# Optimization experiments

Measured on AMD Instinct MI355X. Metric: run time of the kernel, lower is better.

Reference implementation:

```python
import jax, jax.numpy as jnp
import numpy as np

N_HEADS = 16

def setup_inputs() -> dict:
    key = jax.random.key(0)
    k1, k2 = jax.random.split(key)
    qkv = jax.random.normal(k1, (4, 3072, 2048), dtype=jnp.float32)
    encoder_kv = jax.random.normal(k2, (4, 2048, 256), dtype=jnp.float32)
    return {"qkv": qkv, "encoder_kv": encoder_kv}

def reference(qkv, encoder_kv):
    bs, width, length = qkv.shape
    ch = width // (3 * N_HEADS)  # 64
    # [bs*H, 3*ch, T] -> q, k, v each [bs*H, ch, T]
    q, k, v = jnp.split(qkv.reshape(bs * N_HEADS, 3 * ch, length), 3, axis=1)
    # encoder kv: [bs, H*2*ch, S] -> ek, ev each [bs*H, ch, S]
    ek, ev = jnp.split(encoder_kv.reshape(bs * N_HEADS, 2 * ch, -1), 2, axis=1)
    k = jnp.concatenate([ek, k], axis=-1)  # [bs*H, ch, S+T]
    v = jnp.concatenate([ev, v], axis=-1)
    scale = ch ** -0.25  # 1/sqrt(sqrt(ch)), applied to both q and k
    weight = jnp.einsum('bct,bcs->bts', q * scale, k * scale)  # [bs*H, T, S+T]
    weight = jax.nn.softmax(weight.astype(jnp.float32), axis=-1).astype(qkv.dtype)
    a = jnp.einsum('bts,bcs->bct', weight, v)  # [bs*H, ch, T]
    return a.reshape(bs, -1, length)
```

## Files before the change

### kernel.cpp

```cpp
#include <hip/hip_runtime.h>
#include <hip/hip_bf16.h>

typedef __attribute__((ext_vector_type(8))) short bf16x8;
typedef __attribute__((ext_vector_type(4))) float f32x4;
typedef __attribute__((ext_vector_type(4))) unsigned u32x4;
typedef __attribute__((ext_vector_type(2))) unsigned u32x2;

#define T_LEN 2048
#define S_ENC 256
#define QSCALE 0.18033688011112042f

#define BARRIER()                                         \
  do {                                                    \
    asm volatile("s_waitcnt lgkmcnt(0)" ::: "memory");    \
    __builtin_amdgcn_s_barrier();                         \
  } while (0)

__device__ __forceinline__ float exp2_hw(float x) {
#if __has_builtin(__builtin_amdgcn_exp2f)
  return __builtin_amdgcn_exp2f(x);
#else
  float r;
  asm("v_exp_f32 %0, %1" : "=v"(r) : "v"(x));
  return r;
#endif
}

__device__ __forceinline__ unsigned cvt_pk_bf16(float lo, float hi) {
  unsigned r;
  asm("v_cvt_pk_bf16_f32 %0, %1, %2" : "=v"(r) : "v"(lo), "v"(hi));
  return r;
}

__device__ __forceinline__ short f2bf(float x) {
  union { __hip_bfloat16 b; short s; } u;
  u.b = __float2bfloat16(x);
  return u.s;
}

__device__ __forceinline__ int swz(int row, int col) {
  return row * 64 + (col ^ ((row & 7) << 3));
}

union PU { u32x4 u; bf16x8 b; };

template<int STRIDE>
__device__ __forceinline__ void tile_body(
    const float* __restrict__ kb, const float* __restrict__ vb, int s0,
    short* __restrict__ Kt, short* __restrict__ Vt,
    const bf16x8 (&qf)[2][2], f32x4 (&o)[2][4], float (&lp)[2], int tid) {

  const int lane = tid & 63;
  const int ln = lane & 15;
  const int lg = lane >> 4;

  const int ks = tid & 63;
  const int kc = (tid >> 6) * 8;
  float kr[8];
  const float* kp = kb + (size_t)kc * STRIDE + (s0 + ks);
#pragma unroll
  for (int r = 0; r < 8; ++r) kr[r] = kp[(size_t)r * STRIDE];

  const int vg = tid & 15;
  const int vc = tid >> 4;
  const float* vp0 = vb + (size_t)vc * STRIDE + (s0 + 4 * vg);
  f32x4 vr0 = *(const f32x4*)(vp0);
  f32x4 vr1 = *(const f32x4*)(vp0 + (size_t)32 * STRIDE);

  BARRIER();

  u32x4 kw;
#pragma unroll
  for (int r = 0; r < 4; ++r) kw[r] = cvt_pk_bf16(kr[2 * r], kr[2 * r + 1]);
  *(u32x4*)(Kt + swz(ks, kc)) = kw;

  const int vcol = 32 * (vg >> 3) + 8 * (vg & 3) + 4 * ((vg >> 2) & 1);
  u32x2 vw0, vw1;
  vw0[0] = cvt_pk_bf16(vr0[0], vr0[1]);
  vw0[1] = cvt_pk_bf16(vr0[2], vr0[3]);
  *(u32x2*)(Vt + swz(vc, vcol)) = vw0;
  vw1[0] = cvt_pk_bf16(vr1[0], vr1[1]);
  vw1[1] = cvt_pk_bf16(vr1[2], vr1[3]);
  *(u32x2*)(Vt + swz(vc + 32, vcol)) = vw1;

  BARRIER();

  f32x4 sacc[2][4];
#pragma unroll
  for (int qt = 0; qt < 2; ++qt)
#pragma unroll
    for (int mt = 0; mt < 4; ++mt) sacc[qt][mt] = (f32x4){0.f, 0.f, 0.f, 0.f};

#pragma unroll
  for (int mt = 0; mt < 4; ++mt) {
    const int row = 16 * mt + ln;
    const bf16x8 kf0 = *(const bf16x8*)(Kt + swz(row, 8 * lg));
    const bf16x8 kf1 = *(const bf16x8*)(Kt + swz(row, 32 + 8 * lg));
#pragma unroll
    for (int qt = 0; qt < 2; ++qt) {
      sacc[qt][mt] = __builtin_amdgcn_mfma_f32_16x16x32_bf16(kf0, qf[qt][0], sacc[qt][mt], 0, 0, 0);
      sacc[qt][mt] = __builtin_amdgcn_mfma_f32_16x16x32_bf16(kf1, qf[qt][1], sacc[qt][mt], 0, 0, 0);
    }
  }

  PU pfrag[2][2];
#pragma unroll
  for (int qt = 0; qt < 2; ++qt) {
    float pmt[4];
#pragma unroll
    for (int mt = 0; mt < 4; ++mt) {
      float p0 = exp2_hw(sacc[qt][mt][0]);
      float p1 = exp2_hw(sacc[qt][mt][1]);
      float p2 = exp2_hw(sacc[qt][mt][2]);
      float p3 = exp2_hw(sacc[qt][mt][3]);
      pfrag[qt][mt >> 1].u[2 * (mt & 1) + 0] = cvt_pk_bf16(p0, p1);
      pfrag[qt][mt >> 1].u[2 * (mt & 1) + 1] = cvt_pk_bf16(p2, p3);
      pmt[mt] = (p0 + p1) + (p2 + p3);
    }
    lp[qt] += (pmt[0] + pmt[1]) + (pmt[2] + pmt[3]);
  }

#pragma unroll
  for (int sub = 0; sub < 2; ++sub)
#pragma unroll
    for (int ct = 0; ct < 4; ++ct) {
      const bf16x8 vf = *(const bf16x8*)(Vt + swz(16 * ct + ln, 32 * sub + 8 * lg));
#pragma unroll
      for (int qt = 0; qt < 2; ++qt)
        o[qt][ct] = __builtin_amdgcn_mfma_f32_16x16x32_bf16(vf, pfrag[qt][sub].b, o[qt][ct], 0, 0, 0);
    }
}

__global__ __launch_bounds__(512, 4) void attn_kernel(
    const float* __restrict__ qkv, const float* __restrict__ ekv,
    float* __restrict__ out) {
  const int tid = threadIdx.x;
  const int lane = tid & 63;
  const int wave = tid >> 6;
  const int ln = lane & 15;
  const int lg = lane >> 4;

  const int bh = blockIdx.x & 63;
  const int qb = blockIdx.x >> 6;
  const int t0 = qb * 256 + wave * 32;

  const float* qp  = qkv + (size_t)bh * 192 * T_LEN;
  const float* kp  = qp + (size_t)64 * T_LEN;
  const float* vp  = qp + (size_t)128 * T_LEN;
  const float* ekp = ekv + (size_t)bh * 128 * S_ENC;
  const float* evp = ekp + (size_t)64 * S_ENC;

  __shared__ __attribute__((aligned(16))) short Kt[64 * 64];
  __shared__ __attribute__((aligned(16))) short Vt[64 * 64];

  bf16x8 qf[2][2];
#pragma unroll
  for (int qt = 0; qt < 2; ++qt)
#pragma unroll
    for (int kk = 0; kk < 2; ++kk)
#pragma unroll
      for (int j = 0; j < 8; ++j)
        qf[qt][kk][j] =
            f2bf(qp[(size_t)(32 * kk + 8 * lg + j) * T_LEN + (t0 + 16 * qt + ln)] * QSCALE);

  f32x4 o[2][4];
#pragma unroll
  for (int qt = 0; qt < 2; ++qt)
#pragma unroll
    for (int ct = 0; ct < 4; ++ct) o[qt][ct] = (f32x4){0.f, 0.f, 0.f, 0.f};
  float lp[2] = {0.f, 0.f};

  for (int st = 0; st < 4; ++st)
    tile_body<S_ENC>(ekp, evp, 64 * st, Kt, Vt, qf, o, lp, tid);
  for (int st = 0; st < 32; ++st)
    tile_body<T_LEN>(kp, vp, 64 * st, Kt, Vt, qf, o, lp, tid);

#pragma unroll
  for (int qt = 0; qt < 2; ++qt) {
    float l = lp[qt];
    l += __shfl_xor(l, 16);
    l += __shfl_xor(l, 32);
    const float inv = 1.0f / l;
    float* ob = out + (size_t)bh * 64 * T_LEN + (t0 + 16 * qt + ln);
#pragma unroll
    for (int ct = 0; ct < 4; ++ct)
#pragma unroll
      for (int r = 0; r < 4; ++r)
        ob[(size_t)(16 * ct + 4 * lg + r) * T_LEN] = o[qt][ct][r] * inv;
  }
}

extern "C" void kernel_launch(void* const* d_in, const int* in_sizes, int n_in,
                              void* d_out, int out_size, void* d_ws, size_t ws_size,
                              hipStream_t stream) {
  const float* qkv = (const float*)d_in[0];
  const float* ekv = (const float*)d_in[1];
  float* out = (float*)d_out;
  attn_kernel<<<dim3(512), dim3(512), 0, stream>>>(qkv, ekv, out);
}
```

Measured before the change: 98.97 us.

## Double per-wave query rows to 64 to amortize K/V tile staging

Each wave now handles 64 query rows (four 16-row tiles) instead of 32, so a block covers 512 queries and the grid drops from 512 to 256 blocks. Every K/V tile converted into shared memory is reused across twice as many queries, halving global K/V reads and bf16 conversion work per query. Score computation is split into two passes of two query tiles to limit live accumulators. In exchange, register pressure rises (launch bounds lowered from 4 to 2 blocks), and with only 256 blocks the GPU may be under-filled.

```diff
diff --git a/kernel.cpp b/kernel.cpp
--- a/kernel.cpp
+++ b/kernel.cpp
@@ -48,7 +48,7 @@
 __device__ __forceinline__ void tile_body(
     const float* __restrict__ kb, const float* __restrict__ vb, int s0,
     short* __restrict__ Kt, short* __restrict__ Vt,
-    const bf16x8 (&qf)[2][2], f32x4 (&o)[2][4], float (&lp)[2], int tid) {
+    const bf16x8 (&qf)[4][2], f32x4 (&o)[4][4], float (&lp)[4], int tid) {
 
   const int lane = tid & 63;
   const int ln = lane & 15;
@@ -85,53 +85,62 @@
 
   BARRIER();
 
-  f32x4 sacc[2][4];
-#pragma unroll
-  for (int qt = 0; qt < 2; ++qt)
-#pragma unroll
-    for (int mt = 0; mt < 4; ++mt) sacc[qt][mt] = (f32x4){0.f, 0.f, 0.f, 0.f};
-
+  bf16x8 kf[4][2];
 #pragma unroll
   for (int mt = 0; mt < 4; ++mt) {
     const int row = 16 * mt + ln;
-    const bf16x8 kf0 = *(const bf16x8*)(Kt + swz(row, 8 * lg));
-    const bf16x8 kf1 = *(const bf16x8*)(Kt + swz(row, 32 + 8 * lg));
-#pragma unroll
-    for (int qt = 0; qt < 2; ++qt) {
-      sacc[qt][mt] = __builtin_amdgcn_mfma_f32_16x16x32_bf16(kf0, qf[qt][0], sacc[qt][mt], 0, 0, 0);
-      sacc[qt][mt] = __builtin_amdgcn_mfma_f32_16x16x32_bf16(kf1, qf[qt][1], sacc[qt][mt], 0, 0, 0);
+    kf[mt][0] = *(const bf16x8*)(Kt + swz(row, 8 * lg));
+    kf[mt][1] = *(const bf16x8*)(Kt + swz(row, 32 + 8 * lg));
+  }
+
+  PU pfrag[4][2];
+#pragma unroll
+  for (int pr = 0; pr < 2; ++pr) {
+    f32x4 sacc[2][4];
+#pragma unroll
+    for (int q2 = 0; q2 < 2; ++q2)
+#pragma unroll
+      for (int mt = 0; mt < 4; ++mt) sacc[q2][mt] = (f32x4){0.f, 0.f, 0.f, 0.f};
+
+#pragma unroll
+    for (int mt = 0; mt < 4; ++mt)
+#pragma unroll
+      for (int q2 = 0; q2 < 2; ++q2) {
+        const int qt = 2 * pr + q2;
+        sacc[q2][mt] = __builtin_amdgcn_mfma_f32_16x16x32_bf16(kf[mt][0], qf[qt][0], sacc[q2][mt], 0, 0, 0);
+        sacc[q2][mt] = __builtin_amdgcn_mfma_f32_16x16x32_bf16(kf[mt][1], qf[qt][1], sacc[q2][mt], 0, 0, 0);
+      }
+
+#pragma unroll
+    for (int q2 = 0; q2 < 2; ++q2) {
+      const int qt = 2 * pr + q2;
+      float pmt[4];
+#pragma unroll
+      for (int mt = 0; mt < 4; ++mt) {
+        float p0 = exp2_hw(sacc[q2][mt][0]);
+        float p1 = exp2_hw(sacc[q2][mt][1]);
+        float p2 = exp2_hw(sacc[q2][mt][2]);
+        float p3 = exp2_hw(sacc[q2][mt][3]);
+        pfrag[qt][mt >> 1].u[2 * (mt & 1) + 0] = cvt_pk_bf16(p0, p1);
+        pfrag[qt][mt >> 1].u[2 * (mt & 1) + 1] = cvt_pk_bf16(p2, p3);
+        pmt[mt] = (p0 + p1) + (p2 + p3);
+      }
+      lp[qt] += (pmt[0] + pmt[1]) + (pmt[2] + pmt[3]);
     }
   }
 
-  PU pfrag[2][2];
-#pragma unroll
-  for (int qt = 0; qt < 2; ++qt) {
-    float pmt[4];
-#pragma unroll
-    for (int mt = 0; mt < 4; ++mt) {
-      float p0 = exp2_hw(sacc[qt][mt][0]);
-      float p1 = exp2_hw(sacc[qt][mt][1]);
-      float p2 = exp2_hw(sacc[qt][mt][2]);
-      float p3 = exp2_hw(sacc[qt][mt][3]);
-      pfrag[qt][mt >> 1].u[2 * (mt & 1) + 0] = cvt_pk_bf16(p0, p1);
-      pfrag[qt][mt >> 1].u[2 * (mt & 1) + 1] = cvt_pk_bf16(p2, p3);
-      pmt[mt] = (p0 + p1) + (p2 + p3);
-    }
-    lp[qt] += (pmt[0] + pmt[1]) + (pmt[2] + pmt[3]);
-  }
-
 #pragma unroll
   for (int sub = 0; sub < 2; ++sub)
 #pragma unroll
     for (int ct = 0; ct < 4; ++ct) {
       const bf16x8 vf = *(const bf16x8*)(Vt + swz(16 * ct + ln, 32 * sub + 8 * lg));
 #pragma unroll
-      for (int qt = 0; qt < 2; ++qt)
+      for (int qt = 0; qt < 4; ++qt)
         o[qt][ct] = __builtin_amdgcn_mfma_f32_16x16x32_bf16(vf, pfrag[qt][sub].b, o[qt][ct], 0, 0, 0);
     }
 }
 
-__global__ __launch_bounds__(512, 4) void attn_kernel(
+__global__ __launch_bounds__(512, 2) void attn_kernel(
     const float* __restrict__ qkv, const float* __restrict__ ekv,
     float* __restrict__ out) {
   const int tid = threadIdx.x;
@@ -142,7 +151,7 @@
 
   const int bh = blockIdx.x & 63;
   const int qb = blockIdx.x >> 6;
-  const int t0 = qb * 256 + wave * 32;
+  const int t0 = qb * 512 + wave * 64;
 
   const float* qp  = qkv + (size_t)bh * 192 * T_LEN;
   const float* kp  = qp + (size_t)64 * T_LEN;
@@ -153,9 +162,9 @@
   __shared__ __attribute__((aligned(16))) short Kt[64 * 64];
   __shared__ __attribute__((aligned(16))) short Vt[64 * 64];
 
-  bf16x8 qf[2][2];
-#pragma unroll
-  for (int qt = 0; qt < 2; ++qt)
+  bf16x8 qf[4][2];
+#pragma unroll
+  for (int qt = 0; qt < 4; ++qt)
 #pragma unroll
     for (int kk = 0; kk < 2; ++kk)
 #pragma unroll
@@ -163,12 +172,12 @@
         qf[qt][kk][j] =
             f2bf(qp[(size_t)(32 * kk + 8 * lg + j) * T_LEN + (t0 + 16 * qt + ln)] * QSCALE);
 
-  f32x4 o[2][4];
-#pragma unroll
-  for (int qt = 0; qt < 2; ++qt)
+  f32x4 o[4][4];
+#pragma unroll
+  for (int qt = 0; qt < 4; ++qt)
 #pragma unroll
     for (int ct = 0; ct < 4; ++ct) o[qt][ct] = (f32x4){0.f, 0.f, 0.f, 0.f};
-  float lp[2] = {0.f, 0.f};
+  float lp[4] = {0.f, 0.f, 0.f, 0.f};
 
   for (int st = 0; st < 4; ++st)
     tile_body<S_ENC>(ekp, evp, 64 * st, Kt, Vt, qf, o, lp, tid);
@@ -176,7 +185,7 @@
     tile_body<T_LEN>(kp, vp, 64 * st, Kt, Vt, qf, o, lp, tid);
 
 #pragma unroll
-  for (int qt = 0; qt < 2; ++qt) {
+  for (int qt = 0; qt < 4; ++qt) {
     float l = lp[qt];
     l += __shfl_xor(l, 16);
     l += __shfl_xor(l, 32);
@@ -196,5 +205,5 @@
   const float* qkv = (const float*)d_in[0];
   const float* ekv = (const float*)d_in[1];
   float* out = (float*)d_out;
-  attn_kernel<<<dim3(512), dim3(512), 0, stream>>>(qkv, ekv, out);
-}
+  attn_kernel<<<dim3(256), dim3(512), 0, stream>>>(qkv, ekv, out);
+}
```

After: 88.15 us. -10.9%, faster.
